# Kernel optimization log

Hardware: AMD Instinct MI355X
Metric: run time of the kernel (lower is better)

## Reference

```python
import jax, jax.numpy as jnp
import numpy as np

N = 50000      # nodes
E = 800000     # edges (avg degree 16)
D = 128        # d_model
H = 8          # num_heads
DK = D // H    # d_k = 16


def setup_inputs() -> dict:
    key = jax.random.key(0)
    ks = jax.random.split(key, 9)
    scale = np.float32(1.0 / np.sqrt(D))
    return {
        "q": jax.random.normal(ks[0], (N, D), jnp.float32),
        "k": jax.random.normal(ks[1], (N, D), jnp.float32),
        "v": jax.random.normal(ks[2], (N, D), jnp.float32),
        "e": jax.random.normal(ks[3], (E, D), jnp.float32),
        "src": jax.random.randint(ks[4], (E,), 0, N),
        "dst": jax.random.randint(ks[5], (E,), 0, N),
        # nn.Linear(D, D, bias=False) weights, stored as [in, out]
        "Wq": jax.random.normal(ks[6], (D, D), jnp.float32) * scale,
        "Wk": jax.random.normal(ks[7], (D, D), jnp.float32) * scale,
        "Wv": jax.random.normal(ks[8], (D, D), jnp.float32) * scale,
    }


def reference(q, k, v, e, src, dst, Wq, Wk, Wv):
    inv_sqrt_dk = np.float32(1.0 / np.sqrt(DK))
    # node-level V projection, then per-edge gather of src V  -> [E, H, DK]
    Vn = (v @ Wv).reshape(N, H, DK)
    Ve = Vn[src]
    # per-edge Q from dst node, K from (src k + edge feature e)
    Qe = (q[dst] @ Wq).reshape(E, H, DK)
    Ke = ((k[src] + e) @ Wk).reshape(E, H, DK)
    # per-edge HxH score matrix: Q @ K^T / sqrt(d_k), leaky-relu
    s = jnp.einsum("ehd,egd->ehg", Qe, Ke) * inv_sqrt_dk   # [E, H, H]
    s = jax.nn.leaky_relu(s)
    # softmax over last head axis (within each edge, as in reduce_func dim=-1)
    A = jax.nn.softmax(s, axis=-1)
    # per-edge message, heads regrouped -> [E, D]
    He = jnp.einsum("ehg,egd->ehd", A, Ve).reshape(E, D)
    # plain sum over incoming edges per destination node -> [N, D]
    return jax.ops.segment_sum(He, dst, num_segments=N)
```

## Files before the change

### kernel.cpp

```cpp
#include <hip/hip_runtime.h>
#include <hip/hip_bf16.h>
#include <math.h>

#define NN 50000
#define EE 800000
#define DD 128
#define HH 8
#define DKK 16

typedef __attribute__((ext_vector_type(8))) short short8;
typedef __attribute__((ext_vector_type(4))) float f32x4;
typedef __attribute__((ext_vector_type(4))) unsigned short ushort4v;
typedef __attribute__((ext_vector_type(8))) unsigned short ushort8v;

static __device__ __forceinline__ unsigned short f2bf(float x) {
  __hip_bfloat16 h = __float2bfloat16(x);
  return *reinterpret_cast<unsigned short*>(&h);
}
static __device__ __forceinline__ float bf2f(unsigned short u) {
  return __uint_as_float(((unsigned int)u) << 16);
}

__global__ __launch_bounds__(256) void hist_kernel(const int* __restrict__ dst,
                                                   int* __restrict__ cnt) {
  int i4 = blockIdx.x * 256 + threadIdx.x;
  if (i4 < EE / 4) {
    int4 d = *(const int4*)&dst[i4 * 4];
    atomicAdd(&cnt[d.x], 1);
    atomicAdd(&cnt[d.y], 1);
    atomicAdd(&cnt[d.z], 1);
    atomicAdd(&cnt[d.w], 1);
  }
}

#define SCAN_NB ((NN + 1023) / 1024)

__global__ __launch_bounds__(256) void scan1_kernel(const int* __restrict__ cnt,
                                                    int* __restrict__ bsum) {
  __shared__ int red[256];
  const int b = blockIdx.x, t = threadIdx.x;
  const int base = b * 1024 + t * 4;
  int s = 0;
  if (base + 3 < NN) {
    int4 v = *(const int4*)&cnt[base];
    s = v.x + v.y + v.z + v.w;
  } else {
    for (int j = 0; j < 4; ++j) if (base + j < NN) s += cnt[base + j];
  }
  red[t] = s;
  __syncthreads();
  for (int off = 1; off < 256; off <<= 1) {
    int v = (t >= off) ? red[t - off] : 0;
    __syncthreads();
    red[t] += v;
    __syncthreads();
  }
  if (t == 255) bsum[b] = red[255];
}

__global__ __launch_bounds__(64) void scan2_kernel(const int* __restrict__ bsum,
                                                   int* __restrict__ bpre) {
  int t = threadIdx.x;
  int v = (t < SCAN_NB) ? bsum[t] : 0;
  for (int off = 1; off < 64; off <<= 1) {
    int u = __shfl_up(v, off);
    if (t >= off) v += u;
  }
  if (t < SCAN_NB) bpre[t + 1] = v;
  if (t == 0) bpre[0] = 0;
}

__global__ __launch_bounds__(256) void scan3_kernel(const int* __restrict__ cnt,
                                                    const int* __restrict__ bpre,
                                                    int* __restrict__ rowptr) {
  __shared__ int red[256];
  const int b = blockIdx.x, t = threadIdx.x;
  const int base = b * 1024 + t * 4;
  int v0 = 0, v1 = 0, v2 = 0, v3 = 0;
  if (base + 3 < NN) {
    int4 v = *(const int4*)&cnt[base];
    v0 = v.x; v1 = v.y; v2 = v.z; v3 = v.w;
  } else {
    if (base + 0 < NN) v0 = cnt[base + 0];
    if (base + 1 < NN) v1 = cnt[base + 1];
    if (base + 2 < NN) v2 = cnt[base + 2];
    if (base + 3 < NN) v3 = cnt[base + 3];
  }
  red[t] = v0 + v1 + v2 + v3;
  __syncthreads();
  for (int off = 1; off < 256; off <<= 1) {
    int v = (t >= off) ? red[t - off] : 0;
    __syncthreads();
    red[t] += v;
    __syncthreads();
  }
  int r = bpre[b] + ((t == 0) ? 0 : red[t - 1]);
  if (base + 0 < NN) { rowptr[base + 0] = r; r += v0; }
  if (base + 1 < NN) { rowptr[base + 1] = r; r += v1; }
  if (base + 2 < NN) { rowptr[base + 2] = r; r += v2; }
  if (base + 3 < NN) { rowptr[base + 3] = r; }
}

__global__ __launch_bounds__(256) void fill_kernel(const int* __restrict__ dst,
                                                   const int* __restrict__ rowptr,
                                                   int* __restrict__ cur,
                                                   int* __restrict__ perm) {
  int i4 = blockIdx.x * 256 + threadIdx.x;
  if (i4 < EE / 4) {
    int4 dv = *(const int4*)&dst[i4 * 4];
    int d0 = dv.x, d1 = dv.y, d2 = dv.z, d3 = dv.w;
    int s0 = atomicAdd(&cur[d0], 1); perm[rowptr[d0] + s0] = i4 * 4 + 0;
    int s1 = atomicAdd(&cur[d1], 1); perm[rowptr[d1] + s1] = i4 * 4 + 1;
    int s2 = atomicAdd(&cur[d2], 1); perm[rowptr[d2] + s2] = i4 * 4 + 2;
    int s3 = atomicAdd(&cur[d3], 1); perm[rowptr[d3] + s3] = i4 * 4 + 3;
  }
}

__global__ void prep_w_kernel(const float* __restrict__ Wq,
                              const float* __restrict__ Wk,
                              const float* __restrict__ Wv,
                              unsigned short* __restrict__ WqT,
                              unsigned short* __restrict__ WkT,
                              unsigned short* __restrict__ WvT) {
  int c = blockIdx.x & 127;
  int m = blockIdx.x >> 7;
  int j = threadIdx.x;
  const float* W = (m == 0) ? Wq : (m == 1) ? Wk : Wv;
  unsigned short* o = (m == 0) ? WqT : (m == 1) ? WkT : WvT;
  o[j * DD + c] = f2bf(W[c * DD + j]);
}

__global__ __launch_bounds__(256) void conv_k_kernel(const float* __restrict__ k,
                                                     unsigned short* __restrict__ kh) {
  int i8 = blockIdx.x * 256 + threadIdx.x;
  if (i8 < NN * DD / 8) {
    float4 a = *(const float4*)&k[(size_t)i8 * 8];
    float4 b = *(const float4*)&k[(size_t)i8 * 8 + 4];
    ushort8v o = { f2bf(a.x), f2bf(a.y), f2bf(a.z), f2bf(a.w),
                   f2bf(b.x), f2bf(b.y), f2bf(b.z), f2bf(b.w) };
    *(ushort8v*)&kh[(size_t)i8 * 8] = o;
  }
}

__global__ __launch_bounds__(512) void node_proj_kernel(
    const float* __restrict__ q, const float* __restrict__ v,
    const unsigned short* __restrict__ WqT, const unsigned short* __restrict__ WvT,
    unsigned short* __restrict__ Qh, unsigned short* __restrict__ Vh)
{
  __shared__ __align__(16) unsigned short xl[64 * 136];
  const int tid = threadIdx.x;
  const int n0 = blockIdx.x * 64;

  for (int m = 0; m < 2; ++m) {
    const float* x = m ? v : q;
    const unsigned short* WT = m ? WvT : WqT;
    unsigned short* o = m ? Vh : Qh;

    __syncthreads();
    #pragma unroll
    for (int p = 0; p < 4; ++p) {
      int f = p * 512 + tid;
      int i = f >> 5, c4 = f & 31;
      int n = n0 + i;
      float4 t = (n < NN) ? *(const float4*)&x[(size_t)n * DD + c4 * 4]
                          : float4{0.f, 0.f, 0.f, 0.f};
      ushort4v u = { f2bf(t.x), f2bf(t.y), f2bf(t.z), f2bf(t.w) };
      *(ushort4v*)&xl[i * 136 + c4 * 4] = u;
    }
    __syncthreads();

    const int lane = tid & 63, wid = tid >> 6;
    const int rg = wid & 3, cg = wid >> 2;
    const int lr = lane & 15, lg = lane >> 4;

    f32x4 acc0 = {0.f,0.f,0.f,0.f}, acc1 = {0.f,0.f,0.f,0.f};
    f32x4 acc2 = {0.f,0.f,0.f,0.f}, acc3 = {0.f,0.f,0.f,0.f};

    const unsigned short* Ab = &xl[(rg * 16 + lr) * 136];
    const unsigned short* B0 = &WT[(size_t)(cg * 64 +  0 + lr) * DD];
    const unsigned short* B1 = &WT[(size_t)(cg * 64 + 16 + lr) * DD];
    const unsigned short* B2 = &WT[(size_t)(cg * 64 + 32 + lr) * DD];
    const unsigned short* B3 = &WT[(size_t)(cg * 64 + 48 + lr) * DD];

    #pragma unroll
    for (int kk = 0; kk < 4; ++kk) {
      const int kof = kk * 32 + lg * 8;
      short8 a = *(const short8*)(Ab + kof);
      acc0 = __builtin_amdgcn_mfma_f32_16x16x32_bf16(a, *(const short8*)(B0 + kof), acc0, 0, 0, 0);
      acc1 = __builtin_amdgcn_mfma_f32_16x16x32_bf16(a, *(const short8*)(B1 + kof), acc1, 0, 0, 0);
      acc2 = __builtin_amdgcn_mfma_f32_16x16x32_bf16(a, *(const short8*)(B2 + kof), acc2, 0, 0, 0);
      acc3 = __builtin_amdgcn_mfma_f32_16x16x32_bf16(a, *(const short8*)(B3 + kof), acc3, 0, 0, 0);
    }

    const int r0 = rg * 16 + lg * 4;
    const int cb = cg * 64 + lr;
    #pragma unroll
    for (int r = 0; r < 4; ++r) {
      int n = n0 + r0 + r;
      if (n < NN) {
        unsigned short* orow = &o[(size_t)n * DD + cb];
        orow[ 0] = f2bf(acc0[r]);
        orow[16] = f2bf(acc1[r]);
        orow[32] = f2bf(acc2[r]);
        orow[48] = f2bf(acc3[r]);
      }
    }
  }
}

__global__ __launch_bounds__(512, 4) void edge_attn_kernel(
    const unsigned short* __restrict__ kh, const float* __restrict__ e,
    const int* __restrict__ src, const int* __restrict__ dst,
    const int* __restrict__ perm,
    const unsigned short* __restrict__ WkT,
    const unsigned short* __restrict__ Qh, const unsigned short* __restrict__ Vh,
    float* __restrict__ out)
{
  __shared__ __align__(16) unsigned short smem[2 * 128 * 136];
  __shared__ int s_perm[128], s_src[128], s_dst[128];

  unsigned short* kke_l = smem;
  unsigned short* ke_l  = smem + 128 * 136;
  float* He = (float*)smem;

  const int tid = threadIdx.x;
  const size_t e0 = (size_t)blockIdx.x * 128;

  if (tid < 128) {
    int pe = perm[e0 + tid];
    s_perm[tid] = pe;
    s_src[tid] = src[pe];
    s_dst[tid] = dst[pe];
  }
  __syncthreads();

  const int i0 = tid >> 3, i1 = i0 + 64, h = tid & 7;
  const int sn0 = s_src[i0], dn0 = s_dst[i0];
  const int sn1 = s_src[i1], dn1 = s_dst[i1];
  ushort8v qa0 = *(const ushort8v*)&Qh[(size_t)dn0 * DD + h * DKK];
  ushort8v qa1 = *(const ushort8v*)&Qh[(size_t)dn0 * DD + h * DKK + 8];
  ushort8v qb0 = *(const ushort8v*)&Qh[(size_t)dn1 * DD + h * DKK];
  ushort8v qb1 = *(const ushort8v*)&Qh[(size_t)dn1 * DD + h * DKK + 8];

  #pragma unroll
  for (int p = 0; p < 4; ++p) {
    int f = p * 512 + tid;
    int i2 = f >> 4, c8 = f & 15;
    ushort8v kv = *(const ushort8v*)&kh[(size_t)s_src[i2] * DD + c8 * 8];
    float4 ea = *(const float4*)&e[(size_t)s_perm[i2] * DD + c8 * 8];
    float4 eb = *(const float4*)&e[(size_t)s_perm[i2] * DD + c8 * 8 + 4];
    ushort8v o;
    o[0] = f2bf(bf2f(kv[0]) + ea.x);
    o[1] = f2bf(bf2f(kv[1]) + ea.y);
    o[2] = f2bf(bf2f(kv[2]) + ea.z);
    o[3] = f2bf(bf2f(kv[3]) + ea.w);
    o[4] = f2bf(bf2f(kv[4]) + eb.x);
    o[5] = f2bf(bf2f(kv[5]) + eb.y);
    o[6] = f2bf(bf2f(kv[6]) + eb.z);
    o[7] = f2bf(bf2f(kv[7]) + eb.w);
    *(ushort8v*)&kke_l[i2 * 136 + c8 * 8] = o;
  }
  __syncthreads();

  {
    const int lane = tid & 63, wid = tid >> 6;
    const int rgA = wid & 3, rgB = (wid & 3) + 4, cg = wid >> 2;
    const int lr = lane & 15, lg = lane >> 4;

    f32x4 aA0 = {0.f,0.f,0.f,0.f}, aA1 = {0.f,0.f,0.f,0.f};
    f32x4 aA2 = {0.f,0.f,0.f,0.f}, aA3 = {0.f,0.f,0.f,0.f};
    f32x4 aB0 = {0.f,0.f,0.f,0.f}, aB1 = {0.f,0.f,0.f,0.f};
    f32x4 aB2 = {0.f,0.f,0.f,0.f}, aB3 = {0.f,0.f,0.f,0.f};

    const unsigned short* AbA = &kke_l[(rgA * 16 + lr) * 136];
    const unsigned short* AbB = &kke_l[(rgB * 16 + lr) * 136];
    const unsigned short* B0 = &WkT[(size_t)(cg * 64 +  0 + lr) * DD];
    const unsigned short* B1 = &WkT[(size_t)(cg * 64 + 16 + lr) * DD];
    const unsigned short* B2 = &WkT[(size_t)(cg * 64 + 32 + lr) * DD];
    const unsigned short* B3 = &WkT[(size_t)(cg * 64 + 48 + lr) * DD];

    #pragma unroll
    for (int kk = 0; kk < 4; ++kk) {
      const int kof = kk * 32 + lg * 8;
      short8 b0 = *(const short8*)(B0 + kof);
      short8 b1 = *(const short8*)(B1 + kof);
      short8 b2 = *(const short8*)(B2 + kof);
      short8 b3 = *(const short8*)(B3 + kof);
      short8 fA = *(const short8*)(AbA + kof);
      short8 fB = *(const short8*)(AbB + kof);
      aA0 = __builtin_amdgcn_mfma_f32_16x16x32_bf16(fA, b0, aA0, 0, 0, 0);
      aA1 = __builtin_amdgcn_mfma_f32_16x16x32_bf16(fA, b1, aA1, 0, 0, 0);
      aA2 = __builtin_amdgcn_mfma_f32_16x16x32_bf16(fA, b2, aA2, 0, 0, 0);
      aA3 = __builtin_amdgcn_mfma_f32_16x16x32_bf16(fA, b3, aA3, 0, 0, 0);
      aB0 = __builtin_amdgcn_mfma_f32_16x16x32_bf16(fB, b0, aB0, 0, 0, 0);
      aB1 = __builtin_amdgcn_mfma_f32_16x16x32_bf16(fB, b1, aB1, 0, 0, 0);
      aB2 = __builtin_amdgcn_mfma_f32_16x16x32_bf16(fB, b2, aB2, 0, 0, 0);
      aB3 = __builtin_amdgcn_mfma_f32_16x16x32_bf16(fB, b3, aB3, 0, 0, 0);
    }

    const int rA = rgA * 16 + lg * 4;
    const int rB = rgB * 16 + lg * 4;
    const int cb = cg * 64 + lr;
    #pragma unroll
    for (int r = 0; r < 4; ++r) {
      ke_l[(rA + r) * 136 + cb +  0] = f2bf(aA0[r]);
      ke_l[(rA + r) * 136 + cb + 16] = f2bf(aA1[r]);
      ke_l[(rA + r) * 136 + cb + 32] = f2bf(aA2[r]);
      ke_l[(rA + r) * 136 + cb + 48] = f2bf(aA3[r]);
      ke_l[(rB + r) * 136 + cb +  0] = f2bf(aB0[r]);
      ke_l[(rB + r) * 136 + cb + 16] = f2bf(aB1[r]);
      ke_l[(rB + r) * 136 + cb + 32] = f2bf(aB2[r]);
      ke_l[(rB + r) * 136 + cb + 48] = f2bf(aB3[r]);
    }
  }
  __syncthreads();

  float sc0[8], sc1[8];
  {
    #pragma unroll
    for (int g = 0; g < 8; ++g) {
      const ushort8v* kp = (const ushort8v*)&ke_l[i0 * 136 + g * DKK];
      ushort8v k0 = kp[0], k1 = kp[1];
      float a = 0.0f;
      #pragma unroll
      for (int t = 0; t < 8; ++t) a = fmaf(bf2f(qa0[t]), bf2f(k0[t]), a);
      #pragma unroll
      for (int t = 0; t < 8; ++t) a = fmaf(bf2f(qa1[t]), bf2f(k1[t]), a);
      a *= 0.25f;
      sc0[g] = (a >= 0.0f) ? a : 0.01f * a;
    }
    #pragma unroll
    for (int g = 0; g < 8; ++g) {
      const ushort8v* kp = (const ushort8v*)&ke_l[i1 * 136 + g * DKK];
      ushort8v k0 = kp[0], k1 = kp[1];
      float a = 0.0f;
      #pragma unroll
      for (int t = 0; t < 8; ++t) a = fmaf(bf2f(qb0[t]), bf2f(k0[t]), a);
      #pragma unroll
      for (int t = 0; t < 8; ++t) a = fmaf(bf2f(qb1[t]), bf2f(k1[t]), a);
      a *= 0.25f;
      sc1[g] = (a >= 0.0f) ? a : 0.01f * a;
    }
    float mx0 = sc0[0], mx1 = sc1[0];
    #pragma unroll
    for (int g = 1; g < 8; ++g) { mx0 = fmaxf(mx0, sc0[g]); mx1 = fmaxf(mx1, sc1[g]); }
    float su0 = 0.0f, su1 = 0.0f;
    #pragma unroll
    for (int g = 0; g < 8; ++g) {
      sc0[g] = __expf(sc0[g] - mx0); su0 += sc0[g];
      sc1[g] = __expf(sc1[g] - mx1); su1 += sc1[g];
    }
    float r0 = 1.0f / su0, r1 = 1.0f / su1;
    #pragma unroll
    for (int g = 0; g < 8; ++g) { sc0[g] *= r0; sc1[g] *= r1; }
  }
  __syncthreads();

  {
    float he[16];
    #pragma unroll
    for (int d = 0; d < 16; ++d) he[d] = 0.0f;
    #pragma unroll
    for (int g = 0; g < 8; ++g) {
      float a = sc0[g];
      ushort8v v0 = *(const ushort8v*)&Vh[(size_t)sn0 * DD + g * DKK];
      ushort8v v1 = *(const ushort8v*)&Vh[(size_t)sn0 * DD + g * DKK + 8];
      #pragma unroll
      for (int t = 0; t < 8; ++t) {
        he[t]     = fmaf(a, bf2f(v0[t]), he[t]);
        he[8 + t] = fmaf(a, bf2f(v1[t]), he[8 + t]);
      }
    }
    #pragma unroll
    for (int d0 = 0; d0 < 4; ++d0) {
      float4 t = { he[d0 * 4], he[d0 * 4 + 1], he[d0 * 4 + 2], he[d0 * 4 + 3] };
      *(float4*)&He[i0 * 132 + h * DKK + d0 * 4] = t;
    }
    #pragma unroll
    for (int d = 0; d < 16; ++d) he[d] = 0.0f;
    #pragma unroll
    for (int g = 0; g < 8; ++g) {
      float a = sc1[g];
      ushort8v v0 = *(const ushort8v*)&Vh[(size_t)sn1 * DD + g * DKK];
      ushort8v v1 = *(const ushort8v*)&Vh[(size_t)sn1 * DD + g * DKK + 8];
      #pragma unroll
      for (int t = 0; t < 8; ++t) {
        he[t]     = fmaf(a, bf2f(v0[t]), he[t]);
        he[8 + t] = fmaf(a, bf2f(v1[t]), he[8 + t]);
      }
    }
    #pragma unroll
    for (int d0 = 0; d0 < 4; ++d0) {
      float4 t = { he[d0 * 4], he[d0 * 4 + 1], he[d0 * 4 + 2], he[d0 * 4 + 3] };
      *(float4*)&He[i1 * 132 + h * DKK + d0 * 4] = t;
    }
  }
  __syncthreads();

  {
    const int c = tid >> 7, d = tid & 127;
    const int base = c * 32;
    float s = 0.0f;
    int curd = s_dst[base];
    #pragma unroll 8
    for (int j = 0; j < 32; ++j) {
      int i2 = base + j;
      int dn2 = s_dst[i2];
      if (dn2 != curd) {
        atomicAdd(&out[(size_t)curd * DD + d], s);
        s = 0.0f;
        curd = dn2;
      }
      s += He[i2 * 132 + d];
    }
    atomicAdd(&out[(size_t)curd * DD + d], s);
  }
}

extern "C" void kernel_launch(void* const* d_in, const int* in_sizes, int n_in,
                              void* d_out, int out_size, void* d_ws, size_t ws_size,
                              hipStream_t stream) {
  const float* q  = (const float*)d_in[0];
  const float* k  = (const float*)d_in[1];
  const float* v  = (const float*)d_in[2];
  const float* e  = (const float*)d_in[3];
  const int*   src = (const int*)d_in[4];
  const int*   dst = (const int*)d_in[5];
  const float* Wq = (const float*)d_in[6];
  const float* Wk = (const float*)d_in[7];
  const float* Wv = (const float*)d_in[8];

  float* out = (float*)d_out;
  char* wsb = (char*)d_ws;
  unsigned short* Qh  = (unsigned short*)wsb;
  unsigned short* Vh  = Qh + (size_t)NN * DD;
  unsigned short* kh  = Vh + (size_t)NN * DD;
  unsigned short* WqT = kh + (size_t)NN * DD;
  unsigned short* WkT = WqT + DD * DD;
  unsigned short* WvT = WkT + DD * DD;
  int* cnt    = (int*)(WvT + DD * DD);
  int* cur    = cnt + NN;
  int* rowptr = cur + NN;
  int* bsum   = rowptr + NN + 1;
  int* bpre   = bsum + 64;
  int* perm   = bpre + 64;

  hipMemsetAsync(d_out, 0, (size_t)NN * DD * sizeof(float), stream);
  hipMemsetAsync(cnt, 0, 2 * NN * sizeof(int), stream);

  hist_kernel <<<(EE / 4 + 255) / 256, 256, 0, stream>>>(dst, cnt);
  scan1_kernel<<<SCAN_NB, 256, 0, stream>>>(cnt, bsum);
  scan2_kernel<<<1, 64, 0, stream>>>(bsum, bpre);
  scan3_kernel<<<SCAN_NB, 256, 0, stream>>>(cnt, bpre, rowptr);
  fill_kernel <<<(EE / 4 + 255) / 256, 256, 0, stream>>>(dst, rowptr, cur, perm);

  prep_w_kernel<<<3 * DD, DD, 0, stream>>>(Wq, Wk, Wv, WqT, WkT, WvT);
  conv_k_kernel<<<(NN * DD / 8 + 255) / 256, 256, 0, stream>>>(k, kh);
  node_proj_kernel<<<(NN + 63) / 64, 512, 0, stream>>>(q, v, WqT, WvT, Qh, Vh);
  edge_attn_kernel<<<EE / 128, 512, 0, stream>>>(kh, e, src, dst, perm,
                                                 WkT, Qh, Vh, out);
}
```

Measured before the change: 400.8 us.

## Halve edge kernel LDS by reusing one bf16 buffer; fold k conversion into node_proj

The edge attention kernel now reuses a single 128x136 bf16 LDS buffer for K+e, the projected K and the per-edge messages. This cuts shared memory per block roughly in half so more blocks can be resident, at the cost of an extra barrier. Messages are stored as bf16 instead of fp32 before the segmented sum, which adds rounding error. The separate k-to-bf16 conversion kernel is merged into node_proj_kernel to save a launch, and the launch_bounds minimum-blocks hint is dropped.

```diff
diff --git a/kernel.cpp b/kernel.cpp
--- a/kernel.cpp
+++ b/kernel.cpp
@@ -130,26 +130,30 @@
   o[j * DD + c] = f2bf(W[c * DD + j]);
 }
 
-__global__ __launch_bounds__(256) void conv_k_kernel(const float* __restrict__ k,
-                                                     unsigned short* __restrict__ kh) {
-  int i8 = blockIdx.x * 256 + threadIdx.x;
-  if (i8 < NN * DD / 8) {
-    float4 a = *(const float4*)&k[(size_t)i8 * 8];
-    float4 b = *(const float4*)&k[(size_t)i8 * 8 + 4];
-    ushort8v o = { f2bf(a.x), f2bf(a.y), f2bf(a.z), f2bf(a.w),
-                   f2bf(b.x), f2bf(b.y), f2bf(b.z), f2bf(b.w) };
-    *(ushort8v*)&kh[(size_t)i8 * 8] = o;
-  }
-}
-
 __global__ __launch_bounds__(512) void node_proj_kernel(
     const float* __restrict__ q, const float* __restrict__ v,
+    const float* __restrict__ k,
     const unsigned short* __restrict__ WqT, const unsigned short* __restrict__ WvT,
-    unsigned short* __restrict__ Qh, unsigned short* __restrict__ Vh)
+    unsigned short* __restrict__ Qh, unsigned short* __restrict__ Vh,
+    unsigned short* __restrict__ kh)
 {
   __shared__ __align__(16) unsigned short xl[64 * 136];
   const int tid = threadIdx.x;
   const int n0 = blockIdx.x * 64;
+
+  #pragma unroll
+  for (int p = 0; p < 2; ++p) {
+    int f = p * 512 + tid;
+    int i = f >> 4, c8 = f & 15;
+    int n = n0 + i;
+    if (n < NN) {
+      float4 a = *(const float4*)&k[(size_t)n * DD + c8 * 8];
+      float4 b = *(const float4*)&k[(size_t)n * DD + c8 * 8 + 4];
+      ushort8v o = { f2bf(a.x), f2bf(a.y), f2bf(a.z), f2bf(a.w),
+                     f2bf(b.x), f2bf(b.y), f2bf(b.z), f2bf(b.w) };
+      *(ushort8v*)&kh[(size_t)n * DD + c8 * 8] = o;
+    }
+  }
 
   for (int m = 0; m < 2; ++m) {
     const float* x = m ? v : q;
@@ -208,7 +212,7 @@
   }
 }
 
-__global__ __launch_bounds__(512, 4) void edge_attn_kernel(
+__global__ __launch_bounds__(512) void edge_attn_kernel(
     const unsigned short* __restrict__ kh, const float* __restrict__ e,
     const int* __restrict__ src, const int* __restrict__ dst,
     const int* __restrict__ perm,
@@ -216,12 +220,8 @@
     const unsigned short* __restrict__ Qh, const unsigned short* __restrict__ Vh,
     float* __restrict__ out)
 {
-  __shared__ __align__(16) unsigned short smem[2 * 128 * 136];
+  __shared__ __align__(16) unsigned short buf[128 * 136];
   __shared__ int s_perm[128], s_src[128], s_dst[128];
-
-  unsigned short* kke_l = smem;
-  unsigned short* ke_l  = smem + 128 * 136;
-  float* He = (float*)smem;
 
   const int tid = threadIdx.x;
   const size_t e0 = (size_t)blockIdx.x * 128;
@@ -258,7 +258,7 @@
     o[5] = f2bf(bf2f(kv[5]) + eb.y);
     o[6] = f2bf(bf2f(kv[6]) + eb.z);
     o[7] = f2bf(bf2f(kv[7]) + eb.w);
-    *(ushort8v*)&kke_l[i2 * 136 + c8 * 8] = o;
+    *(ushort8v*)&buf[i2 * 136 + c8 * 8] = o;
   }
   __syncthreads();
 
@@ -272,8 +272,8 @@
     f32x4 aB0 = {0.f,0.f,0.f,0.f}, aB1 = {0.f,0.f,0.f,0.f};
     f32x4 aB2 = {0.f,0.f,0.f,0.f}, aB3 = {0.f,0.f,0.f,0.f};
 
-    const unsigned short* AbA = &kke_l[(rgA * 16 + lr) * 136];
-    const unsigned short* AbB = &kke_l[(rgB * 16 + lr) * 136];
+    const unsigned short* AbA = &buf[(rgA * 16 + lr) * 136];
+    const unsigned short* AbB = &buf[(rgB * 16 + lr) * 136];
     const unsigned short* B0 = &WkT[(size_t)(cg * 64 +  0 + lr) * DD];
     const unsigned short* B1 = &WkT[(size_t)(cg * 64 + 16 + lr) * DD];
     const unsigned short* B2 = &WkT[(size_t)(cg * 64 + 32 + lr) * DD];
@@ -298,19 +298,21 @@
       aB3 = __builtin_amdgcn_mfma_f32_16x16x32_bf16(fB, b3, aB3, 0, 0, 0);
     }
 
+    __syncthreads();
+
     const int rA = rgA * 16 + lg * 4;
     const int rB = rgB * 16 + lg * 4;
     const int cb = cg * 64 + lr;
     #pragma unroll
     for (int r = 0; r < 4; ++r) {
-      ke_l[(rA + r) * 136 + cb +  0] = f2bf(aA0[r]);
-      ke_l[(rA + r) * 136 + cb + 16] = f2bf(aA1[r]);
-      ke_l[(rA + r) * 136 + cb + 32] = f2bf(aA2[r]);
-      ke_l[(rA + r) * 136 + cb + 48] = f2bf(aA3[r]);
-      ke_l[(rB + r) * 136 + cb +  0] = f2bf(aB0[r]);
-      ke_l[(rB + r) * 136 + cb + 16] = f2bf(aB1[r]);
-      ke_l[(rB + r) * 136 + cb + 32] = f2bf(aB2[r]);
-      ke_l[(rB + r) * 136 + cb + 48] = f2bf(aB3[r]);
+      buf[(rA + r) * 136 + cb +  0] = f2bf(aA0[r]);
+      buf[(rA + r) * 136 + cb + 16] = f2bf(aA1[r]);
+      buf[(rA + r) * 136 + cb + 32] = f2bf(aA2[r]);
+      buf[(rA + r) * 136 + cb + 48] = f2bf(aA3[r]);
+      buf[(rB + r) * 136 + cb +  0] = f2bf(aB0[r]);
+      buf[(rB + r) * 136 + cb + 16] = f2bf(aB1[r]);
+      buf[(rB + r) * 136 + cb + 32] = f2bf(aB2[r]);
+      buf[(rB + r) * 136 + cb + 48] = f2bf(aB3[r]);
     }
   }
   __syncthreads();
@@ -319,7 +321,7 @@
   {
     #pragma unroll
     for (int g = 0; g < 8; ++g) {
-      const ushort8v* kp = (const ushort8v*)&ke_l[i0 * 136 + g * DKK];
+      const ushort8v* kp = (const ushort8v*)&buf[i0 * 136 + g * DKK];
       ushort8v k0 = kp[0], k1 = kp[1];
       float a = 0.0f;
       #pragma unroll
@@ -331,7 +333,7 @@
     }
     #pragma unroll
     for (int g = 0; g < 8; ++g) {
-      const ushort8v* kp = (const ushort8v*)&ke_l[i1 * 136 + g * DKK];
+      const ushort8v* kp = (const ushort8v*)&buf[i1 * 136 + g * DKK];
       ushort8v k0 = kp[0], k1 = kp[1];
       float a = 0.0f;
       #pragma unroll
@@ -371,11 +373,12 @@
         he[8 + t] = fmaf(a, bf2f(v1[t]), he[8 + t]);
       }
     }
-    #pragma unroll
-    for (int d0 = 0; d0 < 4; ++d0) {
-      float4 t = { he[d0 * 4], he[d0 * 4 + 1], he[d0 * 4 + 2], he[d0 * 4 + 3] };
-      *(float4*)&He[i0 * 132 + h * DKK + d0 * 4] = t;
-    }
+    ushort8v o0, o1;
+    #pragma unroll
+    for (int t = 0; t < 8; ++t) { o0[t] = f2bf(he[t]); o1[t] = f2bf(he[8 + t]); }
+    *(ushort8v*)&buf[i0 * 136 + h * DKK]     = o0;
+    *(ushort8v*)&buf[i0 * 136 + h * DKK + 8] = o1;
+
     #pragma unroll
     for (int d = 0; d < 16; ++d) he[d] = 0.0f;
     #pragma unroll
@@ -390,10 +393,9 @@
       }
     }
     #pragma unroll
-    for (int d0 = 0; d0 < 4; ++d0) {
-      float4 t = { he[d0 * 4], he[d0 * 4 + 1], he[d0 * 4 + 2], he[d0 * 4 + 3] };
-      *(float4*)&He[i1 * 132 + h * DKK + d0 * 4] = t;
-    }
+    for (int t = 0; t < 8; ++t) { o0[t] = f2bf(he[t]); o1[t] = f2bf(he[8 + t]); }
+    *(ushort8v*)&buf[i1 * 136 + h * DKK]     = o0;
+    *(ushort8v*)&buf[i1 * 136 + h * DKK + 8] = o1;
   }
   __syncthreads();
 
@@ -411,7 +413,7 @@
         s = 0.0f;
         curd = dn2;
       }
-      s += He[i2 * 132 + d];
+      s += bf2f(buf[i2 * 136 + d]);
     }
     atomicAdd(&out[(size_t)curd * DD + d], s);
   }
@@ -455,8 +457,8 @@
   fill_kernel <<<(EE / 4 + 255) / 256, 256, 0, stream>>>(dst, rowptr, cur, perm);
 
   prep_w_kernel<<<3 * DD, DD, 0, stream>>>(Wq, Wk, Wv, WqT, WkT, WvT);
-  conv_k_kernel<<<(NN * DD / 8 + 255) / 256, 256, 0, stream>>>(k, kh);
-  node_proj_kernel<<<(NN + 63) / 64, 512, 0, stream>>>(q, v, WqT, WvT, Qh, Vh);
+  node_proj_kernel<<<(NN + 63) / 64, 512, 0, stream>>>(q, v, k, WqT, WvT,
+                                                       Qh, Vh, kh);
   edge_attn_kernel<<<EE / 128, 512, 0, stream>>>(kh, e, src, dst, perm,
                                                  WkT, Qh, Vh, out);
 }
```

Result: no change. 396.0 us (-1.2%).
